# Kernel tuning notes

Hardware: AMD Instinct MI355X
Metric: run time of the kernel (lower is better)

The kernel has to match this reference:

```python
import jax, jax.numpy as jnp
import numpy as np

B, A, T, FIN = 128, 30, 65, 4
HID = 64
H = A * HID            # 1920, LSTM hidden size
L = 2                  # n_layers
BURN_IN_STEPS = 20


def setup_inputs() -> dict:
    key = jax.random.key(0)
    ks = jax.random.split(key, 8)
    def w(k, shape, fan_in):
        # xavier-ish scaling so activations stay bounded over 64 steps
        return jax.random.normal(k, shape, jnp.float32) / np.float32(np.sqrt(fan_in))
    return {
        "inputs": jax.random.normal(ks[0], (B, A, T, FIN), jnp.float32),
        "W1": w(ks[1], (HID, FIN), FIN), "b1": jnp.full((HID,), 0.1, jnp.float32),
        "W2": w(ks[2], (HID, HID), HID), "b2": jnp.full((HID,), 0.1, jnp.float32),
        "Wih": w(ks[3], (L, 4 * H, H), H), "Whh": w(ks[4], (L, 4 * H, H), H),
        "bih": jnp.zeros((L, 4 * H), jnp.float32), "bhh": jnp.zeros((L, 4 * H), jnp.float32),
        "W3": w(ks[5], (H, H), H), "b3": jnp.full((H,), 0.1, jnp.float32),
        "W4": w(ks[6], (A * FIN, H), H), "b4": jnp.full((A * FIN,), 0.1, jnp.float32),
        "prediction_steps": 21,
        "burn_in_steps": BURN_IN_STEPS,
    }


def reference(inputs, W1, b1, W2, b2, Wih, Whh, bih, bhh, W3, b3, W4, b4,
              prediction_steps, burn_in_steps):
    # Faithful to JointLSTM.forward with burn_in=True (the mode used in training/eval):
    # steps <= burn_in_steps feed ground truth, afterwards feed previous prediction.
    b, a, t, fin = inputs.shape
    n_layers = Wih.shape[0]
    xs_t = jnp.moveaxis(inputs, 2, 0)  # [T, B, A, Fin] time-major

    def step(carry, xt):
        h, c, prev = carry            # h,c: [L, B, H]; prev: [B, A, Fin]
        x_gt, tt = xt
        ins = jnp.where(tt <= burn_in_steps, x_gt, prev)
        # per-atom MLP (dropout prob 0.0 / eval -> identity)
        x = jax.nn.relu(ins @ W1.T + b1)          # [B, A, HID]
        x = jax.nn.relu(x @ W2.T + b2)            # [B, A, HID]
        x = x.reshape(b, -1)                      # [B, H]
        # stacked LSTM, single timestep, PyTorch gate order i,f,g,o
        hs, cs = [], []
        for l in range(n_layers):
            gates = x @ Wih[l].T + bih[l] + h[l] @ Whh[l].T + bhh[l]  # [B, 4H]
            i_g, f_g, g_g, o_g = jnp.split(gates, 4, axis=-1)
            c_new = jax.nn.sigmoid(f_g) * c[l] + jax.nn.sigmoid(i_g) * jnp.tanh(g_g)
            h_new = jax.nn.sigmoid(o_g) * jnp.tanh(c_new)
            hs.append(h_new); cs.append(c_new)
            x = h_new
        h = jnp.stack(hs); c = jnp.stack(cs)
        x = jax.nn.relu(x @ W3.T + b3)            # [B, H]
        x = x @ W4.T + b4                         # [B, A*Fout]
        out = x.reshape(b, a, -1) + ins           # residual (ww=False)
        return (h, c, out), out

    h0 = jnp.zeros((n_layers, b, Whh.shape[-1]), inputs.dtype)
    init = (h0, jnp.zeros_like(h0), jnp.zeros((b, a, fin), inputs.dtype))
    _, outs = jax.lax.scan(step, init, (xs_t[:-1], jnp.arange(t - 1)))
    return jnp.moveaxis(outs, 0, 2)  # [B, A, T-1, Fout]
```

## Files before the change

### kernel.cpp

```cpp
#include <hip/hip_runtime.h>
#include <stdint.h>

typedef unsigned short u16;
typedef __attribute__((ext_vector_type(8))) short bf16x8;
typedef __attribute__((ext_vector_type(4))) float f32x4;
typedef __attribute__((ext_vector_type(4))) u16 u16x4;

__device__ __forceinline__ u16 f2bf(float f) {
  union { float f; uint32_t u; } v; v.f = f;
  uint32_t u = v.u;
  uint32_t r = u + 0x7fffu + ((u >> 16) & 1u);
  return (u16)(r >> 16);
}
__device__ __forceinline__ float bf2f(u16 h) {
  union { uint32_t u; float f; } v; v.u = ((uint32_t)h) << 16; return v.f;
}
__device__ __forceinline__ float sigm(float x) { return 1.f / (1.f + __expf(-x)); }
__device__ __forceinline__ float tanhfast(float x) {
  float t = __expf(-2.f * fabsf(x));
  float r = (1.f - t) / (1.f + t);
  return x < 0.f ? -r : r;
}

__global__ __launch_bounds__(256) void k_zero(float* __restrict__ p) {
  p[(size_t)blockIdx.x * 256 + threadIdx.x] = 0.f;
}

__global__ __launch_bounds__(256) void k_repB(const float* __restrict__ Wih,
                                              const float* __restrict__ Whh,
                                              u16* __restrict__ dst) {
  int e8 = blockIdx.x * 256 + threadIdx.x;
  if (e8 >= 7372800) return;
  int lane = e8 & 63;
  int t1 = e8 >> 6;
  int g = t1 & 3;
  int t2 = t1 >> 2;
  int k0 = t2 % 120;
  int t3 = t2 / 120;
  int jb = t3 % 120;
  int l = t3 / 120;
  int ln = lane & 15, quad = lane >> 4;
  int n = g * 1920 + jb * 16 + ln;
  const float* src = (k0 < 60)
      ? (Wih + ((size_t)(l * 7680 + n)) * 1920 + k0 * 32 + quad * 8)
      : (Whh + ((size_t)(l * 7680 + n)) * 1920 + (k0 - 60) * 32 + quad * 8);
  float4 a = ((const float4*)src)[0];
  float4 b = ((const float4*)src)[1];
  u16x4 o0, o1;
  o0[0] = f2bf(a.x); o0[1] = f2bf(a.y); o0[2] = f2bf(a.z); o0[3] = f2bf(a.w);
  o1[0] = f2bf(b.x); o1[1] = f2bf(b.y); o1[2] = f2bf(b.z); o1[3] = f2bf(b.w);
  ((u16x4*)(dst + (size_t)e8 * 8))[0] = o0;
  ((u16x4*)(dst + (size_t)e8 * 8))[1] = o1;
}

__global__ __launch_bounds__(256) void k_repW3(const float* __restrict__ W3,
                                               u16* __restrict__ dst) {
  int e8 = blockIdx.x * 256 + threadIdx.x;
  if (e8 >= 460800) return;
  int lane = e8 & 63;
  int t1 = e8 >> 6;
  int nt = t1 & 3;
  int t2 = t1 >> 2;
  int k0 = t2 % 60;
  int nb = t2 / 60;
  int ln = lane & 15, quad = lane >> 4;
  int n = nb * 64 + nt * 16 + ln;
  const float* src = W3 + (size_t)n * 1920 + k0 * 32 + quad * 8;
  float4 a = ((const float4*)src)[0];
  float4 b = ((const float4*)src)[1];
  u16x4 o0, o1;
  o0[0] = f2bf(a.x); o0[1] = f2bf(a.y); o0[2] = f2bf(a.z); o0[3] = f2bf(a.w);
  o1[0] = f2bf(b.x); o1[1] = f2bf(b.y); o1[2] = f2bf(b.z); o1[3] = f2bf(b.w);
  ((u16x4*)(dst + (size_t)e8 * 8))[0] = o0;
  ((u16x4*)(dst + (size_t)e8 * 8))[1] = o1;
}

__global__ __launch_bounds__(64) void k_mlp(
    const float* __restrict__ inputs, const float* __restrict__ prevb,
    const int* __restrict__ burn,
    const float* __restrict__ W1, const float* __restrict__ b1,
    const float* __restrict__ W2, const float* __restrict__ b2,
    u16* __restrict__ A0, float* __restrict__ insb, int t) {
  __shared__ float h1s[64];
  int ba = blockIdx.x;
  int b = ba / 30, a = ba % 30;
  int j = threadIdx.x;
  bool gt = (t <= *burn);
  const float* src = gt ? (inputs + (((size_t)ba) * 65 + t) * 4)
                        : (prevb + (size_t)ba * 4);
  float i0 = src[0], i1 = src[1], i2 = src[2], i3 = src[3];
  float h1 = b1[j] + i0 * W1[j * 4 + 0] + i1 * W1[j * 4 + 1] +
             i2 * W1[j * 4 + 2] + i3 * W1[j * 4 + 3];
  h1 = fmaxf(h1, 0.f);
  h1s[j] = h1;
  __syncthreads();
  float h2 = b2[j];
  const float* w2r = W2 + j * 64;
#pragma unroll 8
  for (int k = 0; k < 64; ++k) h2 += h1s[k] * w2r[k];
  h2 = fmaxf(h2, 0.f);
  int mh = b >> 6, mloc = b & 63, mt = mloc >> 4, ln2 = mloc & 15;
  int ch = a * 2 + (j >> 5), quad2 = (j >> 3) & 3, jj = j & 7;
  size_t xi = ((size_t)(mh * 180 + ch) * 4 + mt) * 512 + (quad2 * 16 + ln2) * 8 + jj;
  A0[xi] = f2bf(h2);
  if (j < 4) insb[(size_t)ba * 4 + j] = src[j];
}

template <int ITERS>
__device__ __forceinline__ void gemm_pipe(const char* __restrict__ aw,
                                          const char* __restrict__ bw,
                                          int lane_off, f32x4 acc[4][4]) {
  constexpr int D = 5;
  bf16x8 Af[D][4], Bf[D][4];
#pragma unroll
  for (int p = 0; p < D; ++p) {
#pragma unroll
    for (int mt = 0; mt < 4; ++mt)
      Af[p][mt] = *(const bf16x8*)(aw + p * 4096 + mt * 1024 + lane_off);
#pragma unroll
    for (int nt = 0; nt < 4; ++nt)
      Bf[p][nt] = *(const bf16x8*)(bw + p * 4096 + nt * 1024 + lane_off);
  }
  for (int o = 0; o < (ITERS - D) / D; ++o) {
    const char* ap = aw + (size_t)(o + 1) * (D * 4096);
    const char* bp = bw + (size_t)(o + 1) * (D * 4096);
#pragma unroll
    for (int d = 0; d < D; ++d) {
#pragma unroll
      for (int mt = 0; mt < 4; ++mt)
#pragma unroll
        for (int nt = 0; nt < 4; ++nt)
          acc[mt][nt] = __builtin_amdgcn_mfma_f32_16x16x32_bf16(
              Af[d][mt], Bf[d][nt], acc[mt][nt], 0, 0, 0);
#pragma unroll
      for (int mt = 0; mt < 4; ++mt)
        Af[d][mt] = *(const bf16x8*)(ap + d * 4096 + mt * 1024 + lane_off);
#pragma unroll
      for (int nt = 0; nt < 4; ++nt)
        Bf[d][nt] = *(const bf16x8*)(bp + d * 4096 + nt * 1024 + lane_off);
    }
  }
#pragma unroll
  for (int d = 0; d < D; ++d) {
#pragma unroll
    for (int mt = 0; mt < 4; ++mt)
#pragma unroll
      for (int nt = 0; nt < 4; ++nt)
        acc[mt][nt] = __builtin_amdgcn_mfma_f32_16x16x32_bf16(
            Af[d][mt], Bf[d][nt], acc[mt][nt], 0, 0, 0);
  }
}

__global__ __launch_bounds__(256, 1) void k_gates(
    const u16* __restrict__ Atl, const u16* __restrict__ Brep_l,
    const float* __restrict__ bih_l, const float* __restrict__ bhh_l,
    float* __restrict__ c_l, u16* __restrict__ hA, u16* __restrict__ hB,
    int rd_off, int sB) {
  __shared__ float red[4][4][16][64];
  const int tid = threadIdx.x;
  const int w = tid >> 6;
  const int lane = tid & 63;
  const int ln = lane & 15, quad = lane >> 4;
  const int jb = blockIdx.x;
  const int mh = blockIdx.y;
  const int lane_off = lane * 16;

  const char* ax = (const char*)Atl + (size_t)mh * 180 * 4096;
  const char* ah = ax + (size_t)rd_off * 4096;
  const char* aw = (w < 2) ? (ax + (size_t)(30 * w) * 4096)
                           : (ah + (size_t)(30 * (w - 2)) * 4096);
  const char* bw = (const char*)Brep_l + ((size_t)jb * 120 + 30 * w) * 4096;

  f32x4 acc[4][4] = {};
  gemm_pipe<30>(aw, bw, lane_off, acc);

#pragma unroll
  for (int mt = 0; mt < 4; ++mt)
#pragma unroll
    for (int nt = 0; nt < 4; ++nt)
      *(f32x4*)&red[w][nt][ln][mt * 16 + quad * 4] = acc[mt][nt];
  __syncthreads();

  f32x4 g[4];
#pragma unroll
  for (int nt = 0; nt < 4; ++nt) {
    f32x4 s = *(const f32x4*)&red[0][nt][ln][w * 16 + quad * 4];
#pragma unroll
    for (int p = 1; p < 4; ++p) {
      f32x4 tv = *(const f32x4*)&red[p][nt][ln][w * 16 + quad * 4];
      s[0] += tv[0]; s[1] += tv[1]; s[2] += tv[2]; s[3] += tv[3];
    }
    g[nt] = s;
  }

  const int kh = jb * 16 + ln;
  const int chl = kh >> 5, quad2 = (kh >> 3) & 3, jj = kh & 7;
  float bs[4];
#pragma unroll
  for (int gi = 0; gi < 4; ++gi) bs[gi] = bih_l[gi * 1920 + kh] + bhh_l[gi * 1920 + kh];
#pragma unroll
  for (int r = 0; r < 4; ++r) {
    int m = mh * 64 + w * 16 + quad * 4 + r;
    float vi = g[0][r] + bs[0];
    float vf = g[1][r] + bs[1];
    float vg = g[2][r] + bs[2];
    float vo = g[3][r] + bs[3];
    size_t ci = (size_t)m * 1920 + kh;
    float cn = sigm(vf) * c_l[ci] + sigm(vi) * tanhfast(vg);
    float hn = sigm(vo) * tanhfast(cn);
    c_l[ci] = cn;
    u16 hb = f2bf(hn);
    int lane2 = quad2 * 16 + quad * 4 + r;
    size_t hi = ((size_t)(mh * 180 + chl) * 4 + w) * 512 + lane2 * 8 + jj;
    hA[hi] = hb;
    size_t hi2 = ((size_t)(mh * sB + chl) * 4 + w) * 512 + lane2 * 8 + jj;
    hB[hi2] = hb;
  }
}

__global__ __launch_bounds__(256, 1) void k_w3(const u16* __restrict__ A2,
                                               const u16* __restrict__ W3r,
                                               const float* __restrict__ b3,
                                               u16* __restrict__ X3b) {
  __shared__ float red[4][4][16][64];
  const int tid = threadIdx.x;
  const int w = tid >> 6;
  const int lane = tid & 63;
  const int ln = lane & 15, quad = lane >> 4;
  const int nb = blockIdx.x;
  const int mh = blockIdx.y;
  const int lane_off = lane * 16;

  const char* aw = (const char*)A2 + ((size_t)mh * 60 + 15 * w) * 4096;
  const char* bw = (const char*)W3r + ((size_t)nb * 60 + 15 * w) * 4096;

  f32x4 acc[4][4] = {};
  gemm_pipe<15>(aw, bw, lane_off, acc);

#pragma unroll
  for (int mt = 0; mt < 4; ++mt)
#pragma unroll
    for (int nt = 0; nt < 4; ++nt)
      *(f32x4*)&red[w][nt][ln][mt * 16 + quad * 4] = acc[mt][nt];
  __syncthreads();

#pragma unroll
  for (int nt = 0; nt < 4; ++nt) {
    f32x4 s = *(const f32x4*)&red[0][nt][ln][w * 16 + quad * 4];
#pragma unroll
    for (int p = 1; p < 4; ++p) {
      f32x4 tv = *(const f32x4*)&red[p][nt][ln][w * 16 + quad * 4];
      s[0] += tv[0]; s[1] += tv[1]; s[2] += tv[2]; s[3] += tv[3];
    }
    int n = nb * 64 + nt * 16 + ln;
    float bias = b3[n];
#pragma unroll
    for (int r = 0; r < 4; ++r) {
      int m = mh * 64 + w * 16 + quad * 4 + r;
      X3b[(size_t)m * 1920 + n] = f2bf(fmaxf(s[r] + bias, 0.f));
    }
  }
}

__global__ __launch_bounds__(64) void k_w4mlp(
    const u16* __restrict__ x3, const float* __restrict__ W4,
    const float* __restrict__ b4, float* __restrict__ insb,
    const float* __restrict__ inputs, const int* __restrict__ burn,
    const float* __restrict__ W1, const float* __restrict__ b1,
    const float* __restrict__ W2, const float* __restrict__ b2,
    u16* __restrict__ A0, float* __restrict__ outp, int t) {
  __shared__ float h1s[64];
  __shared__ float insv[8];
  const int m = blockIdx.x / 15;
  const int q = blockIdx.x % 15;
  const int lane = threadIdx.x;

  const u16* xr = x3 + (size_t)m * 1920;
  float xv[30];
#pragma unroll
  for (int i = 0; i < 30; ++i) xv[i] = bf2f(xr[lane + 64 * i]);
  float vout = 0.f;
#pragma unroll 1
  for (int pi = 0; pi < 8; ++pi) {
    int pp = q * 8 + pi;
    const float* wr = W4 + (size_t)pp * 1920;
    float s = 0.f;
#pragma unroll
    for (int i = 0; i < 30; ++i) s += xv[i] * wr[lane + 64 * i];
#pragma unroll
    for (int off = 32; off > 0; off >>= 1) s += __shfl_xor(s, off);
    if (lane == pi) vout = s + b4[pp] + insb[(size_t)m * 120 + pp];
  }
  if (lane < 8) {
    int pp = q * 8 + lane;
    outp[(((size_t)m * 30 + (pp >> 2)) * 64 + t) * 4 + (pp & 3)] = vout;
    insv[lane] = vout;
  }
  __syncthreads();

  const bool gt = (t + 1 <= *burn);
  const int j = lane;
#pragma unroll 1
  for (int ai = 0; ai < 2; ++ai) {
    const int a = 2 * q + ai;
    const int ba = m * 30 + a;
    float i0, i1, i2, i3;
    if (gt) {
      const float* src = inputs + ((size_t)ba * 65 + (t + 1)) * 4;
      i0 = src[0]; i1 = src[1]; i2 = src[2]; i3 = src[3];
    } else {
      i0 = insv[ai * 4 + 0]; i1 = insv[ai * 4 + 1];
      i2 = insv[ai * 4 + 2]; i3 = insv[ai * 4 + 3];
    }
    float h1 = b1[j] + i0 * W1[j * 4 + 0] + i1 * W1[j * 4 + 1] +
               i2 * W1[j * 4 + 2] + i3 * W1[j * 4 + 3];
    h1 = fmaxf(h1, 0.f);
    h1s[j] = h1;
    __syncthreads();
    float h2 = b2[j];
    const float* w2r = W2 + j * 64;
#pragma unroll 8
    for (int k = 0; k < 64; ++k) h2 += h1s[k] * w2r[k];
    h2 = fmaxf(h2, 0.f);
    int mh = m >> 6, mloc = m & 63, mt = mloc >> 4, ln2 = mloc & 15;
    int ch = a * 2 + (j >> 5), quad2 = (j >> 3) & 3, jj = j & 7;
    size_t xi = ((size_t)(mh * 180 + ch) * 4 + mt) * 512 + (quad2 * 16 + ln2) * 8 + jj;
    A0[xi] = f2bf(h2);
    if (j < 4) {
      float iv = (j == 0) ? i0 : (j == 1) ? i1 : (j == 2) ? i2 : i3;
      insb[(size_t)ba * 4 + j] = iv;
    }
    __syncthreads();
  }
}

extern "C" void kernel_launch(void* const* d_in, const int* in_sizes, int n_in,
                              void* d_out, int out_size, void* d_ws, size_t ws_size,
                              hipStream_t stream) {
  (void)in_sizes; (void)n_in; (void)out_size;
  const float* inputs = (const float*)d_in[0];
  const float* W1 = (const float*)d_in[1];
  const float* b1 = (const float*)d_in[2];
  const float* W2 = (const float*)d_in[3];
  const float* b2 = (const float*)d_in[4];
  const float* Wih = (const float*)d_in[5];
  const float* Whh = (const float*)d_in[6];
  const float* bih = (const float*)d_in[7];
  const float* bhh = (const float*)d_in[8];
  const float* W3 = (const float*)d_in[9];
  const float* b3 = (const float*)d_in[10];
  const float* W4 = (const float*)d_in[11];
  const float* b4 = (const float*)d_in[12];
  const int* burn = (const int*)d_in[14];
  float* outp = (float*)d_out;
  char* ws = (char*)d_ws;

  float* cbuf = (float*)ws;
  u16* A0 = (u16*)(ws + 1966080);
  u16* A1 = (u16*)(ws + 3440640);
  u16* A2 = (u16*)(ws + 4915200);
  u16* X3b = (u16*)(ws + 5406720);
  float* insb = (float*)(ws + 5898240);
  float* prevb = (float*)(ws + 5959680);
  u16* Brep = (u16*)(ws + 6021120);
  u16* W3r = (u16*)(ws + 123985920);
  if (ws_size < 131358720) return;

  hipLaunchKernelGGL(k_zero, dim3(4800), dim3(256), 0, stream, (float*)ws);
  hipLaunchKernelGGL(k_repB, dim3(28800), dim3(256), 0, stream, Wih, Whh, Brep);
  hipLaunchKernelGGL(k_repW3, dim3(1800), dim3(256), 0, stream, W3, W3r);

  const size_t BrepL = (size_t)120 * 120 * 2048;

  hipLaunchKernelGGL(k_mlp, dim3(3840), dim3(64), 0, stream,
                     inputs, prevb, burn, W1, b1, W2, b2, A0, insb, 0);

  for (int t = 0; t < 64; ++t) {
    int p = t & 1;
    int rd_off = 60 + p * 60;
    int wr_off = 60 + (1 - p) * 60;

    hipLaunchKernelGGL(k_gates, dim3(120, 2), dim3(256), 0, stream,
                       A0, Brep, bih, bhh, cbuf,
                       A0 + (size_t)wr_off * 2048, A1, rd_off, 180);
    hipLaunchKernelGGL(k_gates, dim3(120, 2), dim3(256), 0, stream,
                       A1, Brep + BrepL, bih + 7680, bhh + 7680, cbuf + 245760,
                       A1 + (size_t)wr_off * 2048, A2, rd_off, 60);
    hipLaunchKernelGGL(k_w3, dim3(30, 2), dim3(256), 0, stream, A2, W3r, b3, X3b);
    hipLaunchKernelGGL(k_w4mlp, dim3(1920), dim3(64), 0, stream,
                       X3b, W4, b4, insb, inputs, burn, W1, b1, W2, b2,
                       A0, outp, t);
  }
}
```

Baseline: 5.974 ms.

## Fuse both batch halves into one LSTM gates block to reuse weight fragments

The LSTM gates kernel now computes both 64-row batch halves in a single block, so each loaded weight fragment feeds MFMAs for two accumulator sets. The grid shrinks from 240 to 120 blocks and the shared reduction buffer doubles. The aim is to halve redundant weight-fragment loads per step, since the gate GEMM is weight-streaming bound. In exchange, half as many CUs are occupied, register and LDS pressure rise, and the prefetch depth is set to 3.

```diff
diff --git a/kernel.cpp b/kernel.cpp
--- a/kernel.cpp
+++ b/kernel.cpp
@@ -151,70 +151,132 @@
   }
 }
 
-__global__ __launch_bounds__(256, 1) void k_gates(
+template <int ITERS, int D>
+__device__ __forceinline__ void gemm_pipe2(const char* __restrict__ a0,
+                                           const char* __restrict__ a1,
+                                           const char* __restrict__ bw,
+                                           int lane_off,
+                                           f32x4 acc0[4][4], f32x4 acc1[4][4]) {
+  static_assert((ITERS - D) % D == 0, "pipeline depth");
+  bf16x8 A0f[D][4], A1f[D][4], Bf[D][4];
+#pragma unroll
+  for (int p = 0; p < D; ++p) {
+#pragma unroll
+    for (int mt = 0; mt < 4; ++mt) {
+      A0f[p][mt] = *(const bf16x8*)(a0 + p * 4096 + mt * 1024 + lane_off);
+      A1f[p][mt] = *(const bf16x8*)(a1 + p * 4096 + mt * 1024 + lane_off);
+    }
+#pragma unroll
+    for (int nt = 0; nt < 4; ++nt)
+      Bf[p][nt] = *(const bf16x8*)(bw + p * 4096 + nt * 1024 + lane_off);
+  }
+  for (int o = 0; o < (ITERS - D) / D; ++o) {
+    const char* ap0 = a0 + (size_t)(o + 1) * (D * 4096);
+    const char* ap1 = a1 + (size_t)(o + 1) * (D * 4096);
+    const char* bp = bw + (size_t)(o + 1) * (D * 4096);
+#pragma unroll
+    for (int d = 0; d < D; ++d) {
+#pragma unroll
+      for (int mt = 0; mt < 4; ++mt)
+#pragma unroll
+        for (int nt = 0; nt < 4; ++nt) {
+          acc0[mt][nt] = __builtin_amdgcn_mfma_f32_16x16x32_bf16(
+              A0f[d][mt], Bf[d][nt], acc0[mt][nt], 0, 0, 0);
+          acc1[mt][nt] = __builtin_amdgcn_mfma_f32_16x16x32_bf16(
+              A1f[d][mt], Bf[d][nt], acc1[mt][nt], 0, 0, 0);
+        }
+#pragma unroll
+      for (int mt = 0; mt < 4; ++mt) {
+        A0f[d][mt] = *(const bf16x8*)(ap0 + d * 4096 + mt * 1024 + lane_off);
+        A1f[d][mt] = *(const bf16x8*)(ap1 + d * 4096 + mt * 1024 + lane_off);
+      }
+#pragma unroll
+      for (int nt = 0; nt < 4; ++nt)
+        Bf[d][nt] = *(const bf16x8*)(bp + d * 4096 + nt * 1024 + lane_off);
+    }
+  }
+#pragma unroll
+  for (int d = 0; d < D; ++d) {
+#pragma unroll
+    for (int mt = 0; mt < 4; ++mt)
+#pragma unroll
+      for (int nt = 0; nt < 4; ++nt) {
+        acc0[mt][nt] = __builtin_amdgcn_mfma_f32_16x16x32_bf16(
+            A0f[d][mt], Bf[d][nt], acc0[mt][nt], 0, 0, 0);
+        acc1[mt][nt] = __builtin_amdgcn_mfma_f32_16x16x32_bf16(
+            A1f[d][mt], Bf[d][nt], acc1[mt][nt], 0, 0, 0);
+      }
+  }
+}
+
+__global__ __launch_bounds__(256, 1) void k_gates2(
     const u16* __restrict__ Atl, const u16* __restrict__ Brep_l,
     const float* __restrict__ bih_l, const float* __restrict__ bhh_l,
     float* __restrict__ c_l, u16* __restrict__ hA, u16* __restrict__ hB,
     int rd_off, int sB) {
-  __shared__ float red[4][4][16][64];
+  __shared__ float red[4][4][16][128];
   const int tid = threadIdx.x;
   const int w = tid >> 6;
   const int lane = tid & 63;
   const int ln = lane & 15, quad = lane >> 4;
   const int jb = blockIdx.x;
-  const int mh = blockIdx.y;
   const int lane_off = lane * 16;
 
-  const char* ax = (const char*)Atl + (size_t)mh * 180 * 4096;
-  const char* ah = ax + (size_t)rd_off * 4096;
-  const char* aw = (w < 2) ? (ax + (size_t)(30 * w) * 4096)
-                           : (ah + (size_t)(30 * (w - 2)) * 4096);
+  const size_t choff = (w < 2) ? (size_t)(30 * w) * 4096
+                               : ((size_t)rd_off + 30 * (w - 2)) * 4096;
+  const char* a0 = (const char*)Atl + choff;
+  const char* a1 = (const char*)Atl + (size_t)180 * 4096 + choff;
   const char* bw = (const char*)Brep_l + ((size_t)jb * 120 + 30 * w) * 4096;
 
-  f32x4 acc[4][4] = {};
-  gemm_pipe<30>(aw, bw, lane_off, acc);
+  f32x4 acc0[4][4] = {}, acc1[4][4] = {};
+  gemm_pipe2<30, 3>(a0, a1, bw, lane_off, acc0, acc1);
 
 #pragma unroll
   for (int mt = 0; mt < 4; ++mt)
 #pragma unroll
-    for (int nt = 0; nt < 4; ++nt)
-      *(f32x4*)&red[w][nt][ln][mt * 16 + quad * 4] = acc[mt][nt];
+    for (int nt = 0; nt < 4; ++nt) {
+      *(f32x4*)&red[w][nt][ln][mt * 16 + quad * 4] = acc0[mt][nt];
+      *(f32x4*)&red[w][nt][ln][64 + mt * 16 + quad * 4] = acc1[mt][nt];
+    }
   __syncthreads();
-
-  f32x4 g[4];
-#pragma unroll
-  for (int nt = 0; nt < 4; ++nt) {
-    f32x4 s = *(const f32x4*)&red[0][nt][ln][w * 16 + quad * 4];
-#pragma unroll
-    for (int p = 1; p < 4; ++p) {
-      f32x4 tv = *(const f32x4*)&red[p][nt][ln][w * 16 + quad * 4];
-      s[0] += tv[0]; s[1] += tv[1]; s[2] += tv[2]; s[3] += tv[3];
-    }
-    g[nt] = s;
-  }
 
   const int kh = jb * 16 + ln;
   const int chl = kh >> 5, quad2 = (kh >> 3) & 3, jj = kh & 7;
   float bs[4];
 #pragma unroll
   for (int gi = 0; gi < 4; ++gi) bs[gi] = bih_l[gi * 1920 + kh] + bhh_l[gi * 1920 + kh];
-#pragma unroll
-  for (int r = 0; r < 4; ++r) {
-    int m = mh * 64 + w * 16 + quad * 4 + r;
-    float vi = g[0][r] + bs[0];
-    float vf = g[1][r] + bs[1];
-    float vg = g[2][r] + bs[2];
-    float vo = g[3][r] + bs[3];
-    size_t ci = (size_t)m * 1920 + kh;
-    float cn = sigm(vf) * c_l[ci] + sigm(vi) * tanhfast(vg);
-    float hn = sigm(vo) * tanhfast(cn);
-    c_l[ci] = cn;
-    u16 hb = f2bf(hn);
-    int lane2 = quad2 * 16 + quad * 4 + r;
-    size_t hi = ((size_t)(mh * 180 + chl) * 4 + w) * 512 + lane2 * 8 + jj;
-    hA[hi] = hb;
-    size_t hi2 = ((size_t)(mh * sB + chl) * 4 + w) * 512 + lane2 * 8 + jj;
-    hB[hi2] = hb;
+
+#pragma unroll
+  for (int mh = 0; mh < 2; ++mh) {
+    f32x4 g[4];
+#pragma unroll
+    for (int nt = 0; nt < 4; ++nt) {
+      f32x4 s = *(const f32x4*)&red[0][nt][ln][mh * 64 + w * 16 + quad * 4];
+#pragma unroll
+      for (int p = 1; p < 4; ++p) {
+        f32x4 tv = *(const f32x4*)&red[p][nt][ln][mh * 64 + w * 16 + quad * 4];
+        s[0] += tv[0]; s[1] += tv[1]; s[2] += tv[2]; s[3] += tv[3];
+      }
+      g[nt] = s;
+    }
+#pragma unroll
+    for (int r = 0; r < 4; ++r) {
+      int m = mh * 64 + w * 16 + quad * 4 + r;
+      float vi = g[0][r] + bs[0];
+      float vf = g[1][r] + bs[1];
+      float vg = g[2][r] + bs[2];
+      float vo = g[3][r] + bs[3];
+      size_t ci = (size_t)m * 1920 + kh;
+      float cn = sigm(vf) * c_l[ci] + sigm(vi) * tanhfast(vg);
+      float hn = sigm(vo) * tanhfast(cn);
+      c_l[ci] = cn;
+      u16 hb = f2bf(hn);
+      int lane2 = quad2 * 16 + quad * 4 + r;
+      size_t hi = ((size_t)(mh * 180 + chl) * 4 + w) * 512 + lane2 * 8 + jj;
+      hA[hi] = hb;
+      size_t hi2 = ((size_t)(mh * sB + chl) * 4 + w) * 512 + lane2 * 8 + jj;
+      hB[hi2] = hb;
+    }
   }
 }
 
@@ -380,10 +442,10 @@
     int rd_off = 60 + p * 60;
     int wr_off = 60 + (1 - p) * 60;
 
-    hipLaunchKernelGGL(k_gates, dim3(120, 2), dim3(256), 0, stream,
+    hipLaunchKernelGGL(k_gates2, dim3(120), dim3(256), 0, stream,
                        A0, Brep, bih, bhh, cbuf,
                        A0 + (size_t)wr_off * 2048, A1, rd_off, 180);
-    hipLaunchKernelGGL(k_gates, dim3(120, 2), dim3(256), 0, stream,
+    hipLaunchKernelGGL(k_gates2, dim3(120), dim3(256), 0, stream,
                        A1, Brep + BrepL, bih + 7680, bhh + 7680, cbuf + 245760,
                        A1 + (size_t)wr_off * 2048, A2, rd_off, 60);
     hipLaunchKernelGGL(k_w3, dim3(30, 2), dim3(256), 0, stream, A2, W3r, b3, X3b);
```

Measured after the change: 5.482 ms. -8.2%, faster.

## Repartition gate and W3 GEMMs: warps split N instead of K

Applied to the files above, without the earlier changes.

The LSTM gate kernel now has each block cover both batch halves (grid 120 instead of 120x2). Each warp owns one gate's 16-column tile over the full K range, so every B-weight fragment is reused across both M halves and the cross-warp K-split reduction through shared memory goes away. The W3 kernel is changed the same way: each warp computes its own 16 output columns over the full K, with no LDS reduction and no barrier. The cost is a longer serial K loop per warp, fewer blocks (120 instead of 240) for the gate step, and more register pressure from holding two A fragment sets.

```diff
diff --git a/kernel.cpp b/kernel.cpp
--- a/kernel.cpp
+++ b/kernel.cpp
@@ -106,20 +106,68 @@
   if (j < 4) insb[(size_t)ba * 4 + j] = src[j];
 }
 
-template <int ITERS>
-__device__ __forceinline__ void gemm_pipe(const char* __restrict__ aw,
-                                          const char* __restrict__ bw,
-                                          int lane_off, f32x4 acc[4][4]) {
-  constexpr int D = 5;
-  bf16x8 Af[D][4], Bf[D][4];
+template <int ITERS, int D>
+__device__ __forceinline__ void gemm_pipe_g(const char* __restrict__ a0,
+                                            const char* __restrict__ a1,
+                                            const char* __restrict__ bw,
+                                            int lane_off,
+                                            f32x4 acc0[4], f32x4 acc1[4]) {
+  static_assert((ITERS - D) % D == 0, "pipeline depth");
+  bf16x8 A0f[D][4], A1f[D][4], Bf[D];
+#pragma unroll
+  for (int p = 0; p < D; ++p) {
+#pragma unroll
+    for (int mt = 0; mt < 4; ++mt) {
+      A0f[p][mt] = *(const bf16x8*)(a0 + p * 4096 + mt * 1024 + lane_off);
+      A1f[p][mt] = *(const bf16x8*)(a1 + p * 4096 + mt * 1024 + lane_off);
+    }
+    Bf[p] = *(const bf16x8*)(bw + p * 4096 + lane_off);
+  }
+  for (int o = 0; o < (ITERS - D) / D; ++o) {
+    const char* ap0 = a0 + (size_t)(o + 1) * (D * 4096);
+    const char* ap1 = a1 + (size_t)(o + 1) * (D * 4096);
+    const char* bp = bw + (size_t)(o + 1) * (D * 4096);
+#pragma unroll
+    for (int d = 0; d < D; ++d) {
+#pragma unroll
+      for (int mt = 0; mt < 4; ++mt) {
+        acc0[mt] = __builtin_amdgcn_mfma_f32_16x16x32_bf16(
+            A0f[d][mt], Bf[d], acc0[mt], 0, 0, 0);
+        acc1[mt] = __builtin_amdgcn_mfma_f32_16x16x32_bf16(
+            A1f[d][mt], Bf[d], acc1[mt], 0, 0, 0);
+      }
+#pragma unroll
+      for (int mt = 0; mt < 4; ++mt) {
+        A0f[d][mt] = *(const bf16x8*)(ap0 + d * 4096 + mt * 1024 + lane_off);
+        A1f[d][mt] = *(const bf16x8*)(ap1 + d * 4096 + mt * 1024 + lane_off);
+      }
+      Bf[d] = *(const bf16x8*)(bp + d * 4096 + lane_off);
+    }
+  }
+#pragma unroll
+  for (int d = 0; d < D; ++d) {
+#pragma unroll
+    for (int mt = 0; mt < 4; ++mt) {
+      acc0[mt] = __builtin_amdgcn_mfma_f32_16x16x32_bf16(
+          A0f[d][mt], Bf[d], acc0[mt], 0, 0, 0);
+      acc1[mt] = __builtin_amdgcn_mfma_f32_16x16x32_bf16(
+          A1f[d][mt], Bf[d], acc1[mt], 0, 0, 0);
+    }
+  }
+}
+
+template <int ITERS, int D>
+__device__ __forceinline__ void gemm_pipe_w(const char* __restrict__ aw,
+                                            const char* __restrict__ bw,
+                                            int lane_off, f32x4 acc[4]) {
+  static_assert((ITERS - D) % D == 0, "pipeline depth");
+  bf16x8 Af[D][4], Bf[D];
 #pragma unroll
   for (int p = 0; p < D; ++p) {
 #pragma unroll
     for (int mt = 0; mt < 4; ++mt)
       Af[p][mt] = *(const bf16x8*)(aw + p * 4096 + mt * 1024 + lane_off);
-#pragma unroll
-    for (int nt = 0; nt < 4; ++nt)
-      Bf[p][nt] = *(const bf16x8*)(bw + p * 4096 + nt * 1024 + lane_off);
+    Bf[p] = *(const bf16x8*)(bw + p * 4096 + lane_off);
   }
   for (int o = 0; o < (ITERS - D) / D; ++o) {
     const char* ap = aw + (size_t)(o + 1) * (D * 4096);
@@ -128,101 +176,91 @@
     for (int d = 0; d < D; ++d) {
 #pragma unroll
       for (int mt = 0; mt < 4; ++mt)
-#pragma unroll
-        for (int nt = 0; nt < 4; ++nt)
-          acc[mt][nt] = __builtin_amdgcn_mfma_f32_16x16x32_bf16(
-              Af[d][mt], Bf[d][nt], acc[mt][nt], 0, 0, 0);
+        acc[mt] = __builtin_amdgcn_mfma_f32_16x16x32_bf16(
+            Af[d][mt], Bf[d], acc[mt], 0, 0, 0);
 #pragma unroll
       for (int mt = 0; mt < 4; ++mt)
         Af[d][mt] = *(const bf16x8*)(ap + d * 4096 + mt * 1024 + lane_off);
-#pragma unroll
-      for (int nt = 0; nt < 4; ++nt)
-        Bf[d][nt] = *(const bf16x8*)(bp + d * 4096 + nt * 1024 + lane_off);
+      Bf[d] = *(const bf16x8*)(bp + d * 4096 + lane_off);
     }
   }
 #pragma unroll
   for (int d = 0; d < D; ++d) {
 #pragma unroll
     for (int mt = 0; mt < 4; ++mt)
-#pragma unroll
-      for (int nt = 0; nt < 4; ++nt)
-        acc[mt][nt] = __builtin_amdgcn_mfma_f32_16x16x32_bf16(
-            Af[d][mt], Bf[d][nt], acc[mt][nt], 0, 0, 0);
-  }
-}
-
-__global__ __launch_bounds__(256, 1) void k_gates(
+      acc[mt] = __builtin_amdgcn_mfma_f32_16x16x32_bf16(
+          Af[d][mt], Bf[d], acc[mt], 0, 0, 0);
+  }
+}
+
+__global__ __launch_bounds__(256, 1) void k_gates3(
     const u16* __restrict__ Atl, const u16* __restrict__ Brep_l,
     const float* __restrict__ bih_l, const float* __restrict__ bhh_l,
     float* __restrict__ c_l, u16* __restrict__ hA, u16* __restrict__ hB,
     int rd_off, int sB) {
-  __shared__ float red[4][4][16][64];
+  __shared__ float gsm[16][4][132];
   const int tid = threadIdx.x;
   const int w = tid >> 6;
   const int lane = tid & 63;
   const int ln = lane & 15, quad = lane >> 4;
   const int jb = blockIdx.x;
-  const int mh = blockIdx.y;
   const int lane_off = lane * 16;
 
-  const char* ax = (const char*)Atl + (size_t)mh * 180 * 4096;
-  const char* ah = ax + (size_t)rd_off * 4096;
-  const char* aw = (w < 2) ? (ax + (size_t)(30 * w) * 4096)
-                           : (ah + (size_t)(30 * (w - 2)) * 4096);
-  const char* bw = (const char*)Brep_l + ((size_t)jb * 120 + 30 * w) * 4096;
-
-  f32x4 acc[4][4] = {};
-  gemm_pipe<30>(aw, bw, lane_off, acc);
-
-#pragma unroll
-  for (int mt = 0; mt < 4; ++mt)
-#pragma unroll
-    for (int nt = 0; nt < 4; ++nt)
-      *(f32x4*)&red[w][nt][ln][mt * 16 + quad * 4] = acc[mt][nt];
+  const char* ax0 = (const char*)Atl;
+  const char* ax1 = (const char*)Atl + (size_t)180 * 4096;
+  const char* bw0 = (const char*)Brep_l + ((size_t)jb * 480 + w) * 1024;
+
+  f32x4 acc0[4] = {}, acc1[4] = {};
+  gemm_pipe_g<60, 5>(ax0, ax1, bw0, lane_off, acc0, acc1);
+  gemm_pipe_g<60, 5>(ax0 + (size_t)rd_off * 4096, ax1 + (size_t)rd_off * 4096,
+                     bw0 + (size_t)60 * 4096, lane_off, acc0, acc1);
+
+#pragma unroll
+  for (int mt = 0; mt < 4; ++mt) {
+    *(f32x4*)&gsm[ln][w][mt * 16 + quad * 4] = acc0[mt];
+    *(f32x4*)&gsm[ln][w][64 + mt * 16 + quad * 4] = acc1[mt];
+  }
   __syncthreads();
-
-  f32x4 g[4];
-#pragma unroll
-  for (int nt = 0; nt < 4; ++nt) {
-    f32x4 s = *(const f32x4*)&red[0][nt][ln][w * 16 + quad * 4];
-#pragma unroll
-    for (int p = 1; p < 4; ++p) {
-      f32x4 tv = *(const f32x4*)&red[p][nt][ln][w * 16 + quad * 4];
-      s[0] += tv[0]; s[1] += tv[1]; s[2] += tv[2]; s[3] += tv[3];
-    }
-    g[nt] = s;
-  }
 
   const int kh = jb * 16 + ln;
   const int chl = kh >> 5, quad2 = (kh >> 3) & 3, jj = kh & 7;
   float bs[4];
 #pragma unroll
   for (int gi = 0; gi < 4; ++gi) bs[gi] = bih_l[gi * 1920 + kh] + bhh_l[gi * 1920 + kh];
-#pragma unroll
-  for (int r = 0; r < 4; ++r) {
-    int m = mh * 64 + w * 16 + quad * 4 + r;
-    float vi = g[0][r] + bs[0];
-    float vf = g[1][r] + bs[1];
-    float vg = g[2][r] + bs[2];
-    float vo = g[3][r] + bs[3];
-    size_t ci = (size_t)m * 1920 + kh;
-    float cn = sigm(vf) * c_l[ci] + sigm(vi) * tanhfast(vg);
-    float hn = sigm(vo) * tanhfast(cn);
-    c_l[ci] = cn;
-    u16 hb = f2bf(hn);
-    int lane2 = quad2 * 16 + quad * 4 + r;
-    size_t hi = ((size_t)(mh * 180 + chl) * 4 + w) * 512 + lane2 * 8 + jj;
-    hA[hi] = hb;
-    size_t hi2 = ((size_t)(mh * sB + chl) * 4 + w) * 512 + lane2 * 8 + jj;
-    hB[hi2] = hb;
-  }
-}
-
-__global__ __launch_bounds__(256, 1) void k_w3(const u16* __restrict__ A2,
-                                               const u16* __restrict__ W3r,
-                                               const float* __restrict__ b3,
-                                               u16* __restrict__ X3b) {
-  __shared__ float red[4][4][16][64];
+
+#pragma unroll
+  for (int msub = 0; msub < 2; ++msub) {
+    const int mbase = w * 32 + msub * 16 + quad * 4;
+    f32x4 g[4];
+#pragma unroll
+    for (int gi = 0; gi < 4; ++gi) g[gi] = *(const f32x4*)&gsm[ln][gi][mbase];
+    const int mh = w >> 1;
+    const int mt = (w & 1) * 2 + msub;
+#pragma unroll
+    for (int r = 0; r < 4; ++r) {
+      const int m = mbase + r;
+      float vi = g[0][r] + bs[0];
+      float vf = g[1][r] + bs[1];
+      float vg = g[2][r] + bs[2];
+      float vo = g[3][r] + bs[3];
+      size_t ci = (size_t)m * 1920 + kh;
+      float cn = sigm(vf) * c_l[ci] + sigm(vi) * tanhfast(vg);
+      float hn = sigm(vo) * tanhfast(cn);
+      c_l[ci] = cn;
+      u16 hb = f2bf(hn);
+      int lane2 = quad2 * 16 + quad * 4 + r;
+      size_t hi = ((size_t)(mh * 180 + chl) * 4 + mt) * 512 + lane2 * 8 + jj;
+      hA[hi] = hb;
+      size_t hi2 = ((size_t)(mh * sB + chl) * 4 + mt) * 512 + lane2 * 8 + jj;
+      hB[hi2] = hb;
+    }
+  }
+}
+
+__global__ __launch_bounds__(256) void k_w3b(const u16* __restrict__ A2,
+                                             const u16* __restrict__ W3r,
+                                             const float* __restrict__ b3,
+                                             u16* __restrict__ X3b) {
   const int tid = threadIdx.x;
   const int w = tid >> 6;
   const int lane = tid & 63;
@@ -231,35 +269,21 @@
   const int mh = blockIdx.y;
   const int lane_off = lane * 16;
 
-  const char* aw = (const char*)A2 + ((size_t)mh * 60 + 15 * w) * 4096;
-  const char* bw = (const char*)W3r + ((size_t)nb * 60 + 15 * w) * 4096;
-
-  f32x4 acc[4][4] = {};
-  gemm_pipe<15>(aw, bw, lane_off, acc);
-
+  const char* aw = (const char*)A2 + (size_t)mh * 60 * 4096;
+  const char* bw = (const char*)W3r + ((size_t)nb * 240 + w) * 1024;
+
+  f32x4 acc[4] = {};
+  gemm_pipe_w<60, 4>(aw, bw, lane_off, acc);
+
+  const int n = nb * 64 + w * 16 + ln;
+  const float bias = b3[n];
 #pragma unroll
   for (int mt = 0; mt < 4; ++mt)
 #pragma unroll
-    for (int nt = 0; nt < 4; ++nt)
-      *(f32x4*)&red[w][nt][ln][mt * 16 + quad * 4] = acc[mt][nt];
-  __syncthreads();
-
-#pragma unroll
-  for (int nt = 0; nt < 4; ++nt) {
-    f32x4 s = *(const f32x4*)&red[0][nt][ln][w * 16 + quad * 4];
-#pragma unroll
-    for (int p = 1; p < 4; ++p) {
-      f32x4 tv = *(const f32x4*)&red[p][nt][ln][w * 16 + quad * 4];
-      s[0] += tv[0]; s[1] += tv[1]; s[2] += tv[2]; s[3] += tv[3];
-    }
-    int n = nb * 64 + nt * 16 + ln;
-    float bias = b3[n];
-#pragma unroll
     for (int r = 0; r < 4; ++r) {
-      int m = mh * 64 + w * 16 + quad * 4 + r;
-      X3b[(size_t)m * 1920 + n] = f2bf(fmaxf(s[r] + bias, 0.f));
-    }
-  }
+      int m = mh * 64 + mt * 16 + quad * 4 + r;
+      X3b[(size_t)m * 1920 + n] = f2bf(fmaxf(acc[mt][r] + bias, 0.f));
+    }
 }
 
 __global__ __launch_bounds__(64) void k_w4mlp(
@@ -380,13 +404,13 @@
     int rd_off = 60 + p * 60;
     int wr_off = 60 + (1 - p) * 60;
 
-    hipLaunchKernelGGL(k_gates, dim3(120, 2), dim3(256), 0, stream,
+    hipLaunchKernelGGL(k_gates3, dim3(120), dim3(256), 0, stream,
                        A0, Brep, bih, bhh, cbuf,
                        A0 + (size_t)wr_off * 2048, A1, rd_off, 180);
-    hipLaunchKernelGGL(k_gates, dim3(120, 2), dim3(256), 0, stream,
+    hipLaunchKernelGGL(k_gates3, dim3(120), dim3(256), 0, stream,
                        A1, Brep + BrepL, bih + 7680, bhh + 7680, cbuf + 245760,
                        A1 + (size_t)wr_off * 2048, A2, rd_off, 60);
-    hipLaunchKernelGGL(k_w3, dim3(30, 2), dim3(256), 0, stream, A2, W3r, b3, X3b);
+    hipLaunchKernelGGL(k_w3b, dim3(30, 2), dim3(256), 0, stream, A2, W3r, b3, X3b);
     hipLaunchKernelGGL(k_w4mlp, dim3(1920), dim3(64), 0, stream,
                        X3b, W4, b4, insb, inputs, burn, W1, b1, W2, b2,
                        A0, outp, t);
```

New measurement: 8.121 ms. 1.36x slower.
